# Kernel tuning notes

Measured on AMD Instinct MI355X. Metric: run time of the kernel, lower is better.

## Reference

```python
import jax, jax.numpy as jnp
import numpy as np

D_MODEL = 1024
N_HEADS = 16
HEAD_DIM = D_MODEL // N_HEADS
B, T = 2, 2048


def _rotate_half(x):
    # Faithful to module's _apply_rotary: view (..., D//2, 2), pair -> (-x1, x0)
    xr = x.reshape(*x.shape[:-1], HEAD_DIM // 2, 2)
    rot = jnp.stack([-xr[..., 1], xr[..., 0]], axis=-1)
    return rot.reshape(*x.shape)


def setup_inputs() -> dict:
    key = jax.random.key(0)
    ks = jax.random.split(key, 9)
    s = 1.0 / np.sqrt(D_MODEL)
    return {
        "x": jax.random.normal(ks[0], (B, T, D_MODEL), jnp.float32),
        "Wq": jax.random.normal(ks[1], (D_MODEL, D_MODEL), jnp.float32) * s,
        "bq": jax.random.normal(ks[2], (D_MODEL,), jnp.float32) * 0.02,
        "Wk": jax.random.normal(ks[3], (D_MODEL, D_MODEL), jnp.float32) * s,
        "bk": jax.random.normal(ks[4], (D_MODEL,), jnp.float32) * 0.02,
        "Wv": jax.random.normal(ks[5], (D_MODEL, D_MODEL), jnp.float32) * s,
        "bv": jax.random.normal(ks[6], (D_MODEL,), jnp.float32) * 0.02,
        "Wo": jax.random.normal(ks[7], (D_MODEL, D_MODEL), jnp.float32) * s,
        "bo": jax.random.normal(ks[8], (D_MODEL,), jnp.float32) * 0.02,
    }


def reference(x, Wq, bq, Wk, bk, Wv, bv, Wo, bo):
    b, t, _ = x.shape
    # QKV projections (nn.Linear: x @ W.T + b), split heads -> (B, H, T, Dh)
    def proj(W, bias):
        y = x @ W.T + bias
        return y.reshape(b, t, N_HEADS, HEAD_DIM).transpose(0, 2, 1, 3)

    q = _rotate_half(proj(Wq, bq))
    k = _rotate_half(proj(Wk, bk))
    v = proj(Wv, bv)

    scale = 1.0 / jnp.sqrt(jnp.asarray(HEAD_DIM, x.dtype))
    scores = jnp.einsum('bhqd,bhkd->bhqk', q, k) * scale
    causal = jnp.tril(jnp.ones((t, t), bool))  # (T, T)
    scores = jnp.where(causal, scores, jnp.asarray(-jnp.inf, scores.dtype))
    attn = jax.nn.softmax(scores, axis=-1)
    out = jnp.einsum('bhqk,bhkd->bhqd', attn, v)
    out = out.transpose(0, 2, 1, 3).reshape(b, t, D_MODEL)
    return out @ Wo.T + bo
```

## Files before the change

kernel.cpp:

```cpp
#include <hip/hip_runtime.h>
#include <stdint.h>

#define DM 1024
#define NH 16
#define HD 64
#define BB 2
#define TT 2048
#define MT (BB*TT)

typedef __bf16 bfrag __attribute__((ext_vector_type(8)));
typedef float  f32x4 __attribute__((ext_vector_type(4)));

__device__ __forceinline__ unsigned short f2bf(float f) {
  union { float f; unsigned u; } v; v.f = f;
  unsigned r = v.u + 0x7fffu + ((v.u >> 16) & 1u);
  return (unsigned short)(r >> 16);
}

__device__ __forceinline__ unsigned short f2bf_hw(float f) {
  __bf16 b = (__bf16)f;
  union { __bf16 b; unsigned short u; } v; v.b = b;
  return v.u;
}

__device__ __forceinline__ unsigned int pack2bf(float a, float b) {
  union { __bf16 h[2]; unsigned int u; } v;
  v.h[0] = (__bf16)a; v.h[1] = (__bf16)b;
  return v.u;
}

__device__ __forceinline__ void async16(const void* g, void* l) {
  __builtin_amdgcn_global_load_lds(
      (const __attribute__((address_space(1))) unsigned int*)g,
      (__attribute__((address_space(3))) unsigned int*)l, 16, 0, 0);
}

#define CBAR() do { asm volatile("" ::: "memory"); \
                    __builtin_amdgcn_s_barrier();  \
                    asm volatile("" ::: "memory"); } while (0)

#define QSCALE 0.18033688011112043f
#define M2BIAS 15.869645449778597f

__global__ __launch_bounds__(256) void cvt_kernel(
    const float* __restrict__ x,  const float* __restrict__ Wq,
    const float* __restrict__ Wk, const float* __restrict__ Wv,
    const float* __restrict__ Wo,
    unsigned short* __restrict__ xb, unsigned short* __restrict__ wqkv,
    unsigned short* __restrict__ wob) {
  int i = blockIdx.x * 256 + threadIdx.x;
  const int NX = MT * DM / 4;
  const int NW = DM * DM / 4;
  const float* src; unsigned short* dst; int off;
  if      (i < NX)        { src = x;  dst = xb;              off = i; }
  else if (i < NX + NW)   { src = Wq; dst = wqkv;            off = i - NX; }
  else if (i < NX + 2*NW) { src = Wk; dst = wqkv + DM*DM;    off = i - NX - NW; }
  else if (i < NX + 3*NW) { src = Wv; dst = wqkv + 2*DM*DM;  off = i - NX - 2*NW; }
  else                    { src = Wo; dst = wob;             off = i - NX - 3*NW; }
  float4 v = ((const float4*)src)[off];
  ushort4 o;
  o.x = f2bf(v.x); o.y = f2bf(v.y); o.z = f2bf(v.z); o.w = f2bf(v.w);
  ((ushort4*)dst)[off] = o;
}

__global__ __launch_bounds__(512, 2) void gemm_qkv(
    const unsigned short* __restrict__ A, const unsigned short* __restrict__ Bm,
    const float* __restrict__ bias0, const float* __restrict__ bias1,
    const float* __restrict__ bias2,
    unsigned short* __restrict__ Qo, unsigned short* __restrict__ Ko,
    unsigned short* __restrict__ Vo) {
  const int tid = threadIdx.x;
  const int wave = tid >> 6, lane = tid & 63;
  const int lr = lane & 15, quad = lane >> 4;
  const int flat = blockIdx.x;
  const int s = (flat & 7) * 32 + (flat >> 3);
  const int m0 = (s & 15) * 256, n0 = (s >> 4) * 192;

  __shared__ __align__(16) unsigned short sA[2][2][256 * 32];
  __shared__ __align__(16) unsigned short sB[2][2][192 * 32];

  const f32x4 zero = {0.f, 0.f, 0.f, 0.f};
  f32x4 acc[4][6];
#pragma unroll
  for (int i = 0; i < 4; i++)
#pragma unroll
    for (int j = 0; j < 6; j++) acc[i][j] = zero;

  const int wm = (wave >> 1) * 64, wn = (wave & 1) * 96;

  auto stagePart = [&](int h) {
    if (h >= 64) return;
    const int ts = h >> 2, pi = h & 3;
    const int buf = ts & 1, hk = pi >> 1;
    const int k0 = ts * 64 + (hk << 5);
    if (pi & 1) {
      unsigned short* dst = &sB[buf][hk][0];
      {
        int fb = wave * 512;
        int fl = fb + lane * 8;
        int row = fl >> 5, c = (fl >> 3) & 3;
        async16(Bm + (size_t)(n0 + row) * 1024 + k0 + ((c ^ ((row >> 1) & 3)) << 3),
                dst + fb);
      }
      if (wave < 4) {
        int fb = 4096 + wave * 512;
        int fl = fb + lane * 8;
        int row = fl >> 5, c = (fl >> 3) & 3;
        async16(Bm + (size_t)(n0 + row) * 1024 + k0 + ((c ^ ((row >> 1) & 3)) << 3),
                dst + fb);
      }
    } else {
      unsigned short* dst = &sA[buf][hk][0];
#pragma unroll
      for (int rep = 0; rep < 2; ++rep) {
        int fb = rep * 4096 + wave * 512;
        int fl = fb + lane * 8;
        int row = fl >> 5, c = (fl >> 3) & 3;
        async16(A + (size_t)(m0 + row) * 1024 + k0 + ((c ^ ((row >> 1) & 3)) << 3),
                dst + fb);
      }
    }
  };

#pragma unroll
  for (int h = 0; h < 6; ++h) stagePart(h);
  asm volatile("s_waitcnt vmcnt(6)" ::: "memory");
  CBAR();

  bfrag af[4], bf[3];
#pragma unroll 1
  for (int t = 0; t < 16; ++t) {
    const int buf = t & 1;
    const int P0 = 4 * t;

    auto rdA = [&](int hk) {
#pragma unroll
      for (int i = 0; i < 4; i++) {
        int ra = wm + i * 16 + lr;
        af[i] = *(const bfrag*)&sA[buf][hk][ra * 32 + ((quad ^ ((ra >> 1) & 3)) << 3)];
      }
    };
    auto rdB = [&](int hk, int jh) {
#pragma unroll
      for (int jj = 0; jj < 3; jj++) {
        int rb = wn + (jh * 3 + jj) * 16 + lr;
        bf[jj] = *(const bfrag*)&sB[buf][hk][rb * 32 + ((quad ^ ((rb >> 1) & 3)) << 3)];
      }
    };
    auto domfma = [&](int jh) {
      __builtin_amdgcn_s_setprio(1);
#pragma unroll
      for (int i = 0; i < 4; i++)
#pragma unroll
        for (int jj = 0; jj < 3; jj++)
          acc[i][jh * 3 + jj] = __builtin_amdgcn_mfma_f32_16x16x32_bf16(
              af[i], bf[jj], acc[i][jh * 3 + jj], 0, 0, 0);
      __builtin_amdgcn_s_setprio(0);
    };

    rdA(0); rdB(0, 0);
    stagePart(P0 + 6);
    CBAR();
    domfma(0);
    rdB(0, 1);
    stagePart(P0 + 7);
    if (t == 15) { asm volatile("s_waitcnt vmcnt(0)" ::: "memory"); }
    else         { asm volatile("s_waitcnt vmcnt(6)" ::: "memory"); }
    CBAR();
    domfma(1);
    rdA(1); rdB(1, 0);
    stagePart(P0 + 8);
    CBAR();
    domfma(0);
    rdB(1, 1);
    stagePart(P0 + 9);
    if (t == 14)      { asm volatile("s_waitcnt vmcnt(3)" ::: "memory"); }
    else if (t < 14)  { asm volatile("s_waitcnt vmcnt(6)" ::: "memory"); }
    CBAR();
    domfma(1);
  }

#pragma unroll
  for (int j = 0; j < 6; j++) {
    int n = n0 + wn + j * 16 + lr;
    int qkv = n >> 10, nn = n & 1023;
    float bias = (qkv == 0 ? bias0 : qkv == 1 ? bias1 : bias2)[nn];
    int h = nn >> 6, d = nn & 63;
    if (qkv == 2) {
#pragma unroll
      for (int i = 0; i < 4; i++) {
        int t0 = m0 + wm + i * 16 + quad * 4;
        int b = t0 >> 11, tt = t0 & 2047;
        size_t bb = (size_t)((b << 4) + h) * (TT * 64);
        int kk0 = tt & 63;
        size_t off = bb + (size_t)(tt >> 6) * 4096 +
                     (size_t)((kk0 >> 3) << 9) + (d << 3) + (kk0 & 7);
        ushort4 pk;
        pk.x = f2bf(acc[i][j][0] + bias);
        pk.y = f2bf(acc[i][j][1] + bias);
        pk.z = f2bf(acc[i][j][2] + bias);
        pk.w = f2bf(acc[i][j][3] + bias);
        *(ushort4*)(Vo + off) = pk;
      }
    } else {
#pragma unroll
      for (int i = 0; i < 4; i++)
#pragma unroll
        for (int r = 0; r < 4; r++) {
          int m = m0 + wm + i * 16 + quad * 4 + r;
          float vb = acc[i][j][r] + bias;
          float pv = __shfl_xor(vb, 1);
          float val = (n & 1) ? pv : -pv;
          int b = m >> 11, t = m & 2047;
          size_t base = (size_t)((b << 4) + h) * (TT * 64);
          if (qkv == 0) {
            Qo[base + (size_t)t * 64 + d] = f2bf(val * QSCALE);
          } else {
            int kk = t & 63;
            size_t off = base + (size_t)(t >> 6) * 4096 +
                         (size_t)((d >> 3) << 9) + (kk << 3) + (d & 7);
            Ko[off] = f2bf(val);
          }
        }
    }
  }
}

__global__ __launch_bounds__(256) void gemm_op(
    const unsigned short* __restrict__ A, const unsigned short* __restrict__ Bm,
    const float* __restrict__ bias0, float* __restrict__ Co) {
  const int tid = threadIdx.x;
  const int wave = tid >> 6, lane = tid & 63;
  const int lr = lane & 15, quad = lane >> 4;
  const int m0 = blockIdx.y * 64, n0 = blockIdx.x * 128;
  __shared__ __align__(16) unsigned short sA[2][64 * 64];
  __shared__ __align__(16) unsigned short sB[2][128 * 64];
  const f32x4 zero = {0.f, 0.f, 0.f, 0.f};
  f32x4 acc[2][4];
#pragma unroll
  for (int i = 0; i < 2; i++)
#pragma unroll
    for (int j = 0; j < 4; j++) acc[i][j] = zero;
  const int wm = (wave >> 1) * 32, wn = (wave & 1) * 64;

  auto swz = [](int row) { return ((row & 1) << 2) | ((row >> 1) & 3); };

  auto stage = [&](int kt, int buf) {
    const int k0 = kt * 64;
#pragma unroll
    for (int rep = 0; rep < 2; ++rep) {
      int fb = rep * 2048 + wave * 512;
      int fl = fb + lane * 8;
      int row = fl >> 6, pc = (fl >> 3) & 7;
      async16(A + (size_t)(m0 + row) * 1024 + k0 + ((pc ^ swz(row)) << 3), &sA[buf][fb]);
    }
#pragma unroll
    for (int rep = 0; rep < 4; ++rep) {
      int fb = rep * 2048 + wave * 512;
      int fl = fb + lane * 8;
      int row = fl >> 6, pc = (fl >> 3) & 7;
      async16(Bm + (size_t)(n0 + row) * 1024 + k0 + ((pc ^ swz(row)) << 3), &sB[buf][fb]);
    }
  };

  stage(0, 0);
  for (int kt = 0; kt < 16; ++kt) {
    const int buf = kt & 1;
    __syncthreads();
    if (kt + 1 < 16) stage(kt + 1, buf ^ 1);
#pragma unroll
    for (int ks = 0; ks < 2; ++ks) {
      bfrag af[2], bfr[4];
#pragma unroll
      for (int i = 0; i < 2; i++) {
        int ra = wm + i * 16 + lr;
        af[i] = *(const bfrag*)&sA[buf][ra * 64 + (((ks * 4 + quad) ^ swz(ra)) << 3)];
      }
#pragma unroll
      for (int j = 0; j < 4; j++) {
        int rb = wn + j * 16 + lr;
        bfr[j] = *(const bfrag*)&sB[buf][rb * 64 + (((ks * 4 + quad) ^ swz(rb)) << 3)];
      }
#pragma unroll
      for (int i = 0; i < 2; i++)
#pragma unroll
        for (int j = 0; j < 4; j++)
          acc[i][j] = __builtin_amdgcn_mfma_f32_16x16x32_bf16(af[i], bfr[j], acc[i][j], 0, 0, 0);
    }
  }

#pragma unroll
  for (int j = 0; j < 4; j++) {
    int n = n0 + wn + j * 16 + lr;
    float bias = bias0[n];
#pragma unroll
    for (int i = 0; i < 2; i++)
#pragma unroll
      for (int r = 0; r < 4; r++) {
        int m = m0 + wm + i * 16 + quad * 4 + r;
        Co[(size_t)m * 1024 + n] = acc[i][j][r] + bias;
      }
  }
}

__global__ __launch_bounds__(256, 4) void flash_kernel(
    const unsigned short* __restrict__ Qg, const unsigned short* __restrict__ Kg,
    const unsigned short* __restrict__ Vg, unsigned short* __restrict__ Og) {
  const int flat = blockIdx.x;
  const int xcd = flat & 7;
  const int idx = flat >> 3;
  const int g   = idx >> 5;
  const int bh  = g * 8 + xcd;
  const int a   = idx & 31;
  const int qt  = (g & 1) ? (31 - a) : a;
  const int tid = threadIdx.x, wave = tid >> 6, lane = tid & 63;
  const int lr = lane & 15, quad = lane >> 4;
  __shared__ __align__(16) unsigned short sP[4][1024];
  const size_t base = (size_t)bh * (TT * 64);
  const int nS = qt + 1;
  const int qg = qt * 64 + wave * 16 + lr;
  const f32x4 zero = {0.f, 0.f, 0.f, 0.f};

  bfrag qf0, qf1;
  {
    const unsigned short* qr = Qg + base + (size_t)qg * 64;
    qf0 = *(const bfrag*)(qr + quad * 8);
    qf1 = *(const bfrag*)(qr + 32 + quad * 8);
  }
  f32x4 o[4];
  float rs = 0.f;
#pragma unroll
  for (int j = 0; j < 4; j++) o[j] = zero;

  const unsigned short* kgb = Kg + base;
  const unsigned short* vgb = Vg + base;
  const int lko = quad * 512 + lr * 8;

  const int pwr = lr * 8 + (quad & 1) * 4;
  const int pq2 = quad >> 1;

#pragma unroll 1
  for (int kt = 0; kt < nS; ++kt) {
    const unsigned short* kt_k = kgb + (size_t)kt * 4096;
    const unsigned short* kt_v = vgb + (size_t)kt * 4096;
    bfrag kf0[4], kf1[4], vf0[4], vf1[4];
#pragma unroll
    for (int ct = 0; ct < 4; ct++) {
      kf0[ct] = *(const bfrag*)(kt_k + lko + ct * 128);
      kf1[ct] = *(const bfrag*)(kt_k + 2048 + lko + ct * 128);
    }
#pragma unroll
    for (int j = 0; j < 4; j++) {
      vf0[j] = *(const bfrag*)(kt_v + lko + j * 128);
      vf1[j] = *(const bfrag*)(kt_v + 2048 + lko + j * 128);
    }
    f32x4 sT[4];
    __builtin_amdgcn_s_setprio(1);
#pragma unroll
    for (int ct = 0; ct < 4; ct++) {
      f32x4 t = __builtin_amdgcn_mfma_f32_16x16x32_bf16(kf0[ct], qf0, zero, 0, 0, 0);
      sT[ct]  = __builtin_amdgcn_mfma_f32_16x16x32_bf16(kf1[ct], qf1, t,    0, 0, 0);
    }
    __builtin_amdgcn_s_setprio(0);
    const bool diag = (kt == qt);
#pragma unroll
    for (int ct = 0; ct < 4; ++ct) {
      float e[4];
#pragma unroll
      for (int r = 0; r < 4; ++r)
        e[r] = exp2f(sT[ct][r] - M2BIAS);
      if (diag) {
#pragma unroll
        for (int r = 0; r < 4; ++r) {
          int key = kt * 64 + ct * 16 + quad * 4 + r;
          if (key > qg) e[r] = 0.f;
        }
      }
      rs += (e[0] + e[1]) + (e[2] + e[3]);
      uint2 w;
      w.x = pack2bf(e[0], e[1]);
      w.y = pack2bf(e[2], e[3]);
      *(uint2*)&sP[wave][(ct * 2 + pq2) * 128 + pwr] = w;
    }
    bfrag pf0 = *(const bfrag*)&sP[wave][quad * 128 + lr * 8];
    bfrag pf1 = *(const bfrag*)&sP[wave][(4 + quad) * 128 + lr * 8];
    __builtin_amdgcn_s_setprio(1);
#pragma unroll
    for (int j = 0; j < 4; j++) {
      o[j] = __builtin_amdgcn_mfma_f32_16x16x32_bf16(vf0[j], pf0, o[j], 0, 0, 0);
      o[j] = __builtin_amdgcn_mfma_f32_16x16x32_bf16(vf1[j], pf1, o[j], 0, 0, 0);
    }
    __builtin_amdgcn_s_setprio(0);
  }

  rs += __shfl_xor(rs, 16); rs += __shfl_xor(rs, 32);
  const float inv = 1.0f / rs;

  const int b = bh >> 4, h = bh & 15;
#pragma unroll
  for (int j = 0; j < 4; j++) {
    ushort4 pk;
    pk.x = f2bf_hw(o[j][0] * inv); pk.y = f2bf_hw(o[j][1] * inv);
    pk.z = f2bf_hw(o[j][2] * inv); pk.w = f2bf_hw(o[j][3] * inv);
    int col = h * 64 + j * 16 + quad * 4;
    *(ushort4*)(Og + (size_t)(b * TT + qg) * 1024 + col) = pk;
  }
}

extern "C" void kernel_launch(void* const* d_in, const int* in_sizes, int n_in,
                              void* d_out, int out_size, void* d_ws, size_t ws_size,
                              hipStream_t stream) {
  const float* x  = (const float*)d_in[0];
  const float* Wq = (const float*)d_in[1];
  const float* bq = (const float*)d_in[2];
  const float* Wk = (const float*)d_in[3];
  const float* bk = (const float*)d_in[4];
  const float* Wv = (const float*)d_in[5];
  const float* bv = (const float*)d_in[6];
  const float* Wo = (const float*)d_in[7];
  const float* bo = (const float*)d_in[8];
  float* out = (float*)d_out;

  unsigned short* ws = (unsigned short*)d_ws;
  unsigned short* xb   = ws;
  unsigned short* wqkv = ws + (size_t)4 * 1024 * 1024;
  unsigned short* wob  = ws + (size_t)7 * 1024 * 1024;
  unsigned short* Qb   = ws + (size_t)8 * 1024 * 1024;
  unsigned short* Kb   = ws + (size_t)12 * 1024 * 1024;
  unsigned short* Vb   = ws + (size_t)16 * 1024 * 1024;
  unsigned short* Ob   = ws + (size_t)20 * 1024 * 1024;

  cvt_kernel<<<dim3(8192), dim3(256), 0, stream>>>(x, Wq, Wk, Wv, Wo, xb, wqkv, wob);
  gemm_qkv<<<dim3(256), dim3(512), 0, stream>>>(xb, wqkv, bq, bk, bv, Qb, Kb, Vb);
  flash_kernel<<<dim3(1024), dim3(256), 0, stream>>>(Qb, Kb, Vb, Ob);
  gemm_op<<<dim3(8, 64), dim3(256), 0, stream>>>(Ob, wob, bo, out);
}
```

Before: 187.1 us.

## Restructure output projection GEMM with 128x128 tiles and half-step pipelined loads

The output projection GEMM moves from 64x128 tiles with 4 waves to 128x128 tiles with 8 waves. Each 64-wide K step is split into two 32-wide halves with a deeper async prefetch ring and explicit vmcnt waits. The block index is remapped so tiles are spread across XCDs, and MFMA sections run at raised priority. The goal is more data reuse per tile and better overlap of global loads with MFMA work, at the cost of fewer blocks (256) and more hand-tuned wait counts that must match exactly.

After: 183.2 us. 2.1% less time.

```diff
diff --git a/kernel.cpp b/kernel.cpp
--- a/kernel.cpp
+++ b/kernel.cpp
@@ -226,75 +226,88 @@
   }
 }
 
-__global__ __launch_bounds__(256) void gemm_op(
+__global__ __launch_bounds__(512, 2) void gemm_op(
     const unsigned short* __restrict__ A, const unsigned short* __restrict__ Bm,
     const float* __restrict__ bias0, float* __restrict__ Co) {
   const int tid = threadIdx.x;
   const int wave = tid >> 6, lane = tid & 63;
   const int lr = lane & 15, quad = lane >> 4;
-  const int m0 = blockIdx.y * 64, n0 = blockIdx.x * 128;
-  __shared__ __align__(16) unsigned short sA[2][64 * 64];
-  __shared__ __align__(16) unsigned short sB[2][128 * 64];
+  const int flat = blockIdx.x;
+  const int s = (flat & 7) * 32 + (flat >> 3);
+  const int m0 = (s >> 3) * 128, n0 = (s & 7) * 128;
+
+  __shared__ __align__(16) unsigned short sA[2][2][128 * 32];
+  __shared__ __align__(16) unsigned short sB[2][2][128 * 32];
+
   const f32x4 zero = {0.f, 0.f, 0.f, 0.f};
-  f32x4 acc[2][4];
-#pragma unroll
-  for (int i = 0; i < 2; i++)
-#pragma unroll
-    for (int j = 0; j < 4; j++) acc[i][j] = zero;
-  const int wm = (wave >> 1) * 32, wn = (wave & 1) * 64;
-
-  auto swz = [](int row) { return ((row & 1) << 2) | ((row >> 1) & 3); };
-
-  auto stage = [&](int kt, int buf) {
-    const int k0 = kt * 64;
-#pragma unroll
-    for (int rep = 0; rep < 2; ++rep) {
-      int fb = rep * 2048 + wave * 512;
-      int fl = fb + lane * 8;
-      int row = fl >> 6, pc = (fl >> 3) & 7;
-      async16(A + (size_t)(m0 + row) * 1024 + k0 + ((pc ^ swz(row)) << 3), &sA[buf][fb]);
-    }
-#pragma unroll
-    for (int rep = 0; rep < 4; ++rep) {
-      int fb = rep * 2048 + wave * 512;
-      int fl = fb + lane * 8;
-      int row = fl >> 6, pc = (fl >> 3) & 7;
-      async16(Bm + (size_t)(n0 + row) * 1024 + k0 + ((pc ^ swz(row)) << 3), &sB[buf][fb]);
-    }
+  f32x4 acc[4][2];
+#pragma unroll
+  for (int i = 0; i < 4; i++)
+#pragma unroll
+    for (int j = 0; j < 2; j++) acc[i][j] = zero;
+
+  const int wm = (wave >> 2) * 64, wn = (wave & 3) * 32;
+
+  auto stagePart = [&](int h) {
+    if (h >= 32) return;
+    const int ts = h >> 1, hk = h & 1;
+    const int buf = ts & 1;
+    const int k0 = ts * 64 + (hk << 5);
+    int fb = wave * 512;
+    int fl = fb + lane * 8;
+    int row = fl >> 5, c = (fl >> 3) & 3;
+    int col = (c ^ ((row >> 1) & 3)) << 3;
+    async16(A  + (size_t)(m0 + row) * 1024 + k0 + col, &sA[buf][hk][fb]);
+    async16(Bm + (size_t)(n0 + row) * 1024 + k0 + col, &sB[buf][hk][fb]);
   };
 
-  stage(0, 0);
-  for (int kt = 0; kt < 16; ++kt) {
-    const int buf = kt & 1;
-    __syncthreads();
-    if (kt + 1 < 16) stage(kt + 1, buf ^ 1);
-#pragma unroll
-    for (int ks = 0; ks < 2; ++ks) {
-      bfrag af[2], bfr[4];
-#pragma unroll
-      for (int i = 0; i < 2; i++) {
+#pragma unroll
+  for (int h = 0; h < 3; ++h) stagePart(h);
+  asm volatile("s_waitcnt vmcnt(4)" ::: "memory");
+  CBAR();
+
+#pragma unroll 1
+  for (int t = 0; t < 16; ++t) {
+    const int buf = t & 1;
+#pragma unroll
+    for (int hk = 0; hk < 2; ++hk) {
+      bfrag af[4], bfr[2];
+#pragma unroll
+      for (int i = 0; i < 4; i++) {
         int ra = wm + i * 16 + lr;
-        af[i] = *(const bfrag*)&sA[buf][ra * 64 + (((ks * 4 + quad) ^ swz(ra)) << 3)];
-      }
-#pragma unroll
-      for (int j = 0; j < 4; j++) {
-        int rb = wn + j * 16 + lr;
-        bfr[j] = *(const bfrag*)&sB[buf][rb * 64 + (((ks * 4 + quad) ^ swz(rb)) << 3)];
-      }
-#pragma unroll
-      for (int i = 0; i < 2; i++)
-#pragma unroll
-        for (int j = 0; j < 4; j++)
-          acc[i][j] = __builtin_amdgcn_mfma_f32_16x16x32_bf16(af[i], bfr[j], acc[i][j], 0, 0, 0);
-    }
-  }
-
-#pragma unroll
-  for (int j = 0; j < 4; j++) {
+        af[i] = *(const bfrag*)&sA[buf][hk][ra * 32 + ((quad ^ ((ra >> 1) & 3)) << 3)];
+      }
+#pragma unroll
+      for (int jj = 0; jj < 2; jj++) {
+        int rb = wn + jj * 16 + lr;
+        bfr[jj] = *(const bfrag*)&sB[buf][hk][rb * 32 + ((quad ^ ((rb >> 1) & 3)) << 3)];
+      }
+      stagePart(2 * t + hk + 3);
+      if (hk == 0) {
+        if (t < 15) { asm volatile("s_waitcnt vmcnt(4)" ::: "memory"); }
+        else        { asm volatile("s_waitcnt vmcnt(0)" ::: "memory"); }
+      } else {
+        if (t < 14)       { asm volatile("s_waitcnt vmcnt(4)" ::: "memory"); }
+        else if (t == 14) { asm volatile("s_waitcnt vmcnt(2)" ::: "memory"); }
+      }
+      CBAR();
+      __builtin_amdgcn_s_setprio(1);
+#pragma unroll
+      for (int i = 0; i < 4; i++)
+#pragma unroll
+        for (int jj = 0; jj < 2; jj++)
+          acc[i][jj] = __builtin_amdgcn_mfma_f32_16x16x32_bf16(
+              af[i], bfr[jj], acc[i][jj], 0, 0, 0);
+      __builtin_amdgcn_s_setprio(0);
+    }
+  }
+
+#pragma unroll
+  for (int j = 0; j < 2; j++) {
     int n = n0 + wn + j * 16 + lr;
     float bias = bias0[n];
 #pragma unroll
-    for (int i = 0; i < 2; i++)
+    for (int i = 0; i < 4; i++)
 #pragma unroll
       for (int r = 0; r < 4; r++) {
         int m = m0 + wm + i * 16 + quad * 4 + r;
@@ -433,5 +446,5 @@
   cvt_kernel<<<dim3(8192), dim3(256), 0, stream>>>(x, Wq, Wk, Wv, Wo, xb, wqkv, wob);
   gemm_qkv<<<dim3(256), dim3(512), 0, stream>>>(xb, wqkv, bq, bk, bv, Qb, Kb, Vb);
   flash_kernel<<<dim3(1024), dim3(256), 0, stream>>>(Qb, Kb, Vb, Ob);
-  gemm_op<<<dim3(8, 64), dim3(256), 0, stream>>>(Ob, wob, bo, out);
-}
+  gemm_op<<<dim3(256), dim3(512), 0, stream>>>(Ob, wob, bo, out);
+}
```
